# Kernel tuning notes

Hardware: AMD Instinct MI355X
Metric: run time of the kernel (lower is better)

The kernel has to match this reference:

```python
import jax, jax.numpy as jnp
import numpy as np

B, D, H, NL, DFF, N = 64, 768, 12, 12, 3072, 197
HD = D // H  # 64
SCALE = HD ** -0.5


def setup_inputs() -> dict:
    key = jax.random.key(0)
    ks = iter(jax.random.split(key, 64))
    def rn(shape, s=0.02):
        return jax.random.normal(next(ks), shape, jnp.float32) * s
    inp = {
        'x': jax.random.normal(next(ks), (B, 12, 1000), jnp.float32),
        # PatchEmbed convs (torch Conv1d weight layout OIH)
        'conv1_w': rn((256, 12, 5), 0.1), 'conv1_b': jnp.zeros((256,), jnp.float32),
        'bn1_g': jnp.ones((256,), jnp.float32), 'bn1_b': jnp.zeros((256,), jnp.float32),
        'bn1_m': jnp.zeros((256,), jnp.float32), 'bn1_v': jnp.ones((256,), jnp.float32),
        'conv2_w': rn((768, 256, 5), 0.05), 'conv2_b': jnp.zeros((768,), jnp.float32),
        'bn2_g': jnp.ones((768,), jnp.float32), 'bn2_b': jnp.zeros((768,), jnp.float32),
        'bn2_m': jnp.zeros((768,), jnp.float32), 'bn2_v': jnp.ones((768,), jnp.float32),
        'cls_token': rn((1, 1, D)), 'pos_embed': rn((1, N, D)),
        # 12 transformer blocks, stacked. Linear weights stored [in, out].
        'ln1_g': jnp.ones((NL, D), jnp.float32), 'ln1_b': jnp.zeros((NL, D), jnp.float32),
        'qkv_w': rn((NL, D, 3 * D)),            # qkv_bias=False
        'proj_w': rn((NL, D, D)), 'proj_b': jnp.zeros((NL, D), jnp.float32),
        'ln2_g': jnp.ones((NL, D), jnp.float32), 'ln2_b': jnp.zeros((NL, D), jnp.float32),
        'fc1_w': rn((NL, D, DFF)), 'fc1_b': jnp.zeros((NL, DFF), jnp.float32),
        'fc2_w': rn((NL, DFF, D)), 'fc2_b': jnp.zeros((NL, D), jnp.float32),
        'norm_g': jnp.ones((D,), jnp.float32), 'norm_b': jnp.zeros((D,), jnp.float32),
        # ProjectionHead (nonlinear): Linear(768->768,no bias)+BN, ReLU, Linear(768->512,no bias)+BN
        'p1_w': rn((D, D)),
        'p1bn_g': jnp.ones((D,), jnp.float32), 'p1bn_b': jnp.zeros((D,), jnp.float32),
        'p1bn_m': jnp.zeros((D,), jnp.float32), 'p1bn_v': jnp.ones((D,), jnp.float32),
        'p2_w': rn((D, 512)),
        'p2bn_g': jnp.ones((512,), jnp.float32), 'p2bn_b': jnp.zeros((512,), jnp.float32),
        'p2bn_m': jnp.zeros((512,), jnp.float32), 'p2bn_v': jnp.ones((512,), jnp.float32),
    }
    return inp


def _conv1d(x, w, b, stride):
    y = jax.lax.conv_general_dilated(x, w, (stride,), 'VALID',
                                     dimension_numbers=('NCH', 'OIH', 'NCH'))
    return y + b[None, :, None]


def _bn_c(x, g, b, m, v, eps=1e-5):  # BatchNorm1d eval, channel axis 1 of (B,C,L)
    return (x - m[None, :, None]) * (g[None, :, None] / jnp.sqrt(v[None, :, None] + eps)) + b[None, :, None]


def _bn_f(x, g, b, m, v, eps=1e-5):  # BatchNorm1d eval on (B,F)
    return (x - m) * (g / jnp.sqrt(v + eps)) + b


def _ln(x, g, b, eps=1e-6):
    mu = x.mean(-1, keepdims=True)
    var = jnp.var(x, axis=-1, keepdims=True)
    return (x - mu) * jax.lax.rsqrt(var + eps) * g + b


def reference(x, conv1_w, conv1_b, bn1_g, bn1_b, bn1_m, bn1_v,
              conv2_w, conv2_b, bn2_g, bn2_b, bn2_m, bn2_v,
              cls_token, pos_embed,
              ln1_g, ln1_b, qkv_w, proj_w, proj_b,
              ln2_g, ln2_b, fc1_w, fc1_b, fc2_w, fc2_b,
              norm_g, norm_b,
              p1_w, p1bn_g, p1bn_b, p1bn_m, p1bn_v,
              p2_w, p2bn_g, p2bn_b, p2bn_m, p2bn_v):
    # PatchEmbed: conv -> ReLU -> BN, twice; then (B, 196, 768)
    h = _bn_c(jax.nn.relu(_conv1d(x, conv1_w, conv1_b, 5)), bn1_g, bn1_b, bn1_m, bn1_v)
    h = _bn_c(jax.nn.relu(_conv1d(h, conv2_w, conv2_b, 1)), bn2_g, bn2_b, bn2_m, bn2_v)
    h = jnp.transpose(h, (0, 2, 1))  # [B, 196, D]
    b = h.shape[0]
    tok = jnp.concatenate([jnp.broadcast_to(cls_token, (b, 1, D)), h], axis=1) + pos_embed  # [B, 197, D]

    for i in range(NL):
        y = _ln(tok, ln1_g[i], ln1_b[i])
        qkv = jnp.einsum('bnd,de->bne', y, qkv_w[i]).reshape(b, N, 3, H, HD)
        q, k, v = jnp.moveaxis(qkv, 2, 0)  # each [B, N, H, HD]
        q = jnp.transpose(q, (0, 2, 1, 3)) * SCALE  # [B, H, N, HD]
        k = jnp.transpose(k, (0, 2, 1, 3))
        v = jnp.transpose(v, (0, 2, 1, 3))
        attn = jax.nn.softmax(jnp.einsum('bhnd,bhmd->bhnm', q, k), axis=-1)
        o = jnp.einsum('bhnm,bhmd->bhnd', attn, v)
        o = jnp.transpose(o, (0, 2, 1, 3)).reshape(b, N, D)
        tok = tok + jnp.einsum('bnd,de->bne', o, proj_w[i]) + proj_b[i]
        y = _ln(tok, ln2_g[i], ln2_b[i])
        y = jax.nn.gelu(jnp.einsum('bnd,df->bnf', y, fc1_w[i]) + fc1_b[i], approximate=False)
        tok = tok + jnp.einsum('bnf,fd->bnd', y, fc2_w[i]) + fc2_b[i]

    cls = _ln(tok, norm_g, norm_b)[:, 0]  # global_pool='token'
    z = _bn_f(cls @ p1_w, p1bn_g, p1bn_b, p1bn_m, p1bn_v)
    z = jax.nn.relu(z)
    z = _bn_f(z @ p2_w, p2bn_g, p2bn_b, p2bn_m, p2bn_v)
    return z
```

## Files before the change

### kernel.cpp

```cpp
#include <hip/hip_runtime.h>
#include <hip/hip_bf16.h>

typedef __hip_bfloat16 bf16;
typedef __attribute__((ext_vector_type(8))) short bf16x8;
typedef __attribute__((ext_vector_type(4))) float f32x4;

__device__ __forceinline__ float bf2f(bf16 v) { return __bfloat162float(v); }
__device__ __forceinline__ unsigned short f2bfu(float f) {
    bf16 h = __float2bfloat16(f);
    return __builtin_bit_cast(unsigned short, h);
}

__device__ __forceinline__ void gload16(const void* g, void* lds) {
    __builtin_amdgcn_global_load_lds(
        (const __attribute__((address_space(1))) unsigned int*)g,
        (__attribute__((address_space(3))) unsigned int*)lds, 16, 0, 0);
}

__device__ __forceinline__ float gelu_f(float x) {
    float u = 0.7978845608f * (x + 0.044715f * x * x * x);
    float e = __expf(-2.0f * fabsf(u));
    float th = (1.f - e) / (1.f + e);
    th = u < 0.f ? -th : th;
    return 0.5f * x * (1.f + th);
}

__global__ __launch_bounds__(256)
void conv1_kernel(const float* __restrict__ x, const float* __restrict__ w,
                  const float* __restrict__ bias,
                  const float* __restrict__ g, const float* __restrict__ b,
                  const float* __restrict__ m, const float* __restrict__ v,
                  bf16* __restrict__ h1) {
    int bo = blockIdx.x;
    int bb = bo >> 8, o = bo & 255;
    int l = threadIdx.x;
    if (l >= 200) return;
    const float* wo = w + o * 60;
    const float* xb = x + bb * 12000;
    float acc = bias[o];
#pragma unroll
    for (int i = 0; i < 12; i++)
#pragma unroll
        for (int t = 0; t < 5; t++)
            acc = fmaf(xb[i * 1000 + 5 * l + t], wo[i * 5 + t], acc);
    acc = fmaxf(acc, 0.f);
    float sc = g[o] * rsqrtf(v[o] + 1e-5f);
    acc = (acc - m[o]) * sc + b[o];
    h1[bo * 200 + l] = __float2bfloat16(acc);
}

__global__ __launch_bounds__(256)
void im2col_kernel(const bf16* __restrict__ h1, bf16* __restrict__ A2) {
    int idx = blockIdx.x * 256 + threadIdx.x;
    int row = idx / 1280, c = idx - row * 1280;
    int bb = row / 196, l = row - bb * 196;
    int i = c / 5, t = c - i * 5;
    A2[idx] = h1[(bb * 256 + i) * 200 + l + t];
}

__global__ __launch_bounds__(256)
void add_cls_pos(const float* __restrict__ cls, const float* __restrict__ pos,
                 float* __restrict__ tok) {
    int idx = blockIdx.x * 256 + threadIdx.x;
    int bb = idx / 768, d = idx - bb * 768;
    tok[(size_t)bb * 197 * 768 + d] = cls[d] + pos[d];
}

__global__ __launch_bounds__(256)
void cvt_kernel(const float* __restrict__ in, bf16* __restrict__ out, int n) {
    int idx = blockIdx.x * 256 + threadIdx.x;
    if (idx < n) out[idx] = __float2bfloat16(in[idx]);
}

__global__ __launch_bounds__(256)
void wtrans_layer(const float* __restrict__ qkvw, const float* __restrict__ projw,
                  const float* __restrict__ fc1w, const float* __restrict__ fc2w,
                  bf16* __restrict__ qkvT, bf16* __restrict__ projT,
                  bf16* __restrict__ fc1T, bf16* __restrict__ fc2T) {
    __shared__ float tile[32][33];
    int blk = blockIdx.x;
    const float* in; bf16* out; int Kd, Nd, t0;
    if (blk < 1728)      { in = qkvw; out = qkvT; Kd = 768;  Nd = 2304; t0 = blk; }
    else if (blk < 2304) { in = projw; out = projT; Kd = 768;  Nd = 768;  t0 = blk - 1728; }
    else if (blk < 4608) { in = fc1w; out = fc1T; Kd = 768;  Nd = 3072; t0 = blk - 2304; }
    else                 { in = fc2w; out = fc2T; Kd = 3072; Nd = 768;  t0 = blk - 4608; }
    int ntiles = Nd >> 5;
    int kt = t0 / ntiles, nt = t0 - kt * ntiles;
    int k0 = kt * 32, n0 = nt * 32;
    int tx = threadIdx.x & 31, ty = threadIdx.x >> 5;
#pragma unroll
    for (int j = 0; j < 4; j++)
        tile[ty + 8 * j][tx] = in[(size_t)(k0 + ty + 8 * j) * Nd + n0 + tx];
    __syncthreads();
#pragma unroll
    for (int j = 0; j < 4; j++)
        out[(size_t)(n0 + ty + 8 * j) * Kd + k0 + tx] = __float2bfloat16(tile[tx][ty + 8 * j]);
}

__global__ __launch_bounds__(256)
void wtrans2(const float* __restrict__ in, bf16* __restrict__ out, int Kd, int Nd) {
    __shared__ float tile[32][33];
    int ntiles = Nd >> 5;
    int kt = blockIdx.x / ntiles, nt = blockIdx.x - kt * ntiles;
    int k0 = kt * 32, n0 = nt * 32;
    int tx = threadIdx.x & 31, ty = threadIdx.x >> 5;
#pragma unroll
    for (int j = 0; j < 4; j++)
        tile[ty + 8 * j][tx] = in[(size_t)(k0 + ty + 8 * j) * Nd + n0 + tx];
    __syncthreads();
#pragma unroll
    for (int j = 0; j < 4; j++)
        out[(size_t)(n0 + ty + 8 * j) * Kd + k0 + tx] = __float2bfloat16(tile[tx][ty + 8 * j]);
}

__global__ __launch_bounds__(256)
void ln_kernel(const float* __restrict__ x, bf16* __restrict__ y,
               const float* __restrict__ g, const float* __restrict__ b,
               int nrows, int xstride) {
    int row = blockIdx.x * 4 + (threadIdx.x >> 6);
    if (row >= nrows) return;
    int l = threadIdx.x & 63;
    const float* xr = x + (size_t)row * xstride;
    float4 v0 = *(const float4*)(xr + l * 4);
    float4 v1 = *(const float4*)(xr + 256 + l * 4);
    float4 v2 = *(const float4*)(xr + 512 + l * 4);
    float s1 = 0.f, s2 = 0.f;
    {
        float e;
        e = v0.x; s1 += e; s2 += e * e;  e = v0.y; s1 += e; s2 += e * e;
        e = v0.z; s1 += e; s2 += e * e;  e = v0.w; s1 += e; s2 += e * e;
        e = v1.x; s1 += e; s2 += e * e;  e = v1.y; s1 += e; s2 += e * e;
        e = v1.z; s1 += e; s2 += e * e;  e = v1.w; s1 += e; s2 += e * e;
        e = v2.x; s1 += e; s2 += e * e;  e = v2.y; s1 += e; s2 += e * e;
        e = v2.z; s1 += e; s2 += e * e;  e = v2.w; s1 += e; s2 += e * e;
    }
#pragma unroll
    for (int off = 1; off < 64; off <<= 1) {
        s1 += __shfl_xor(s1, off);
        s2 += __shfl_xor(s2, off);
    }
    float mu = s1 * (1.f / 768.f);
    float rs = rsqrtf(s2 * (1.f / 768.f) - mu * mu + 1e-6f);
    bf16* yr = y + (size_t)row * 768;
#pragma unroll
    for (int sgi = 0; sgi < 3; sgi++) {
        float4 vv = sgi == 0 ? v0 : (sgi == 1 ? v1 : v2);
        float4 gg = *(const float4*)(g + sgi * 256 + l * 4);
        float4 bb = *(const float4*)(b + sgi * 256 + l * 4);
        ushort4 o;
        o.x = f2bfu((vv.x - mu) * rs * gg.x + bb.x);
        o.y = f2bfu((vv.y - mu) * rs * gg.y + bb.y);
        o.z = f2bfu((vv.z - mu) * rs * gg.z + bb.z);
        o.w = f2bfu((vv.w - mu) * rs * gg.w + bb.w);
        *(ushort4*)(yr + sgi * 256 + l * 4) = o;
    }
}

enum { E_BF16 = 0, E_RESID = 1, E_GELU = 2, E_CONV2 = 3, E_HEAD1 = 4, E_HEAD2 = 5 };

template<int EPI>
__global__ __launch_bounds__(256)
void gemm2(const bf16* __restrict__ A, const bf16* __restrict__ Bt,
           int M, int N, int K,
           const float* __restrict__ bias,
           bf16* __restrict__ Co, float* __restrict__ tok,
           const float* __restrict__ bng, const float* __restrict__ bnb,
           const float* __restrict__ bnm, const float* __restrict__ bnv,
           const float* __restrict__ pos) {
    __shared__ bf16 As[128 * 64];
    __shared__ bf16 Bs[128 * 64];
    const int t = threadIdx.x;
    const int l = t & 63, w = t >> 6;
    const int wm = (w >> 1) * 64, wn = (w & 1) * 64;

    const int gx = gridDim.x;
    const int nwg = gx * gridDim.y;
    const int d = blockIdx.y * gx + blockIdx.x;
    const int q = nwg >> 3, r = nwg & 7;
    const int xcd = d & 7, pos_ = d >> 3;
    const int lid = (xcd < r ? xcd * (q + 1) : r * (q + 1) + (xcd - r) * q) + pos_;
    const int row0 = (lid / gx) * 128, col0 = (lid % gx) * 128;

    const int lr = l & 15, kg = l >> 4;

    const int srow = w * 8 + (l >> 3);
    const int sc = ((l & 7) ^ (l >> 3)) * 8;
    const int dstoff = w * 1024 + l * 16;

    const f32x4 zero4 = {0.f, 0.f, 0.f, 0.f};
    f32x4 acc[4][4];
#pragma unroll
    for (int i = 0; i < 4; i++)
#pragma unroll
        for (int j = 0; j < 4; j++) acc[i][j] = zero4;

    for (int k0 = 0; k0 < K; k0 += 64) {
#pragma unroll
        for (int p = 0; p < 4; p++) {
            int rr = srow + p * 32;
            int gra = row0 + rr; if (gra >= M) gra = M - 1;
            gload16(A + (size_t)gra * K + k0 + sc, (char*)As + p * 4096 + dstoff);
            gload16(Bt + (size_t)(col0 + rr) * K + k0 + sc, (char*)Bs + p * 4096 + dstoff);
        }
        __syncthreads();
#pragma unroll
        for (int ks = 0; ks < 2; ks++) {
            bf16x8 af[4], bfv[4];
            const int cc = ((ks * 4 + kg) ^ (lr & 7)) * 16;
#pragma unroll
            for (int i = 0; i < 4; i++) {
                af[i]  = *(const bf16x8*)((const char*)As + (wm + i * 16 + lr) * 128 + cc);
                bfv[i] = *(const bf16x8*)((const char*)Bs + (wn + i * 16 + lr) * 128 + cc);
            }
#pragma unroll
            for (int i = 0; i < 4; i++)
#pragma unroll
                for (int j = 0; j < 4; j++)
                    acc[i][j] = __builtin_amdgcn_mfma_f32_16x16x32_bf16(af[i], bfv[j], acc[i][j], 0, 0, 0);
        }
        __syncthreads();
    }

    const int rbase = row0 + wm + (kg << 2);
#pragma unroll
    for (int i = 0; i < 4; i++) {
#pragma unroll
        for (int sr = 0; sr < 4; sr++) {
            int rr = rbase + i * 16 + sr;
            if (rr < M) {
#pragma unroll
                for (int j = 0; j < 4; j++) {
                    int c = col0 + wn + j * 16 + lr;
                    float vv = acc[i][j][sr];
                    if (EPI == E_BF16) {
                        Co[(size_t)rr * N + c] = __float2bfloat16(vv);
                    } else if (EPI == E_RESID) {
                        float* p = tok + (size_t)rr * N + c;
                        *p += vv + bias[c];
                    } else if (EPI == E_GELU) {
                        Co[(size_t)rr * N + c] = __float2bfloat16(gelu_f(vv + bias[c]));
                    } else if (EPI == E_CONV2) {
                        float xx = vv + bias[c];
                        xx = fmaxf(xx, 0.f);
                        float sc2 = bng[c] * rsqrtf(bnv[c] + 1e-5f);
                        xx = (xx - bnm[c]) * sc2 + bnb[c];
                        int bb = rr / 196, ll = rr - bb * 196;
                        xx += pos[(size_t)(1 + ll) * 768 + c];
                        tok[(size_t)(bb * 197 + 1 + ll) * 768 + c] = xx;
                    } else if (EPI == E_HEAD1) {
                        float sc2 = bng[c] * rsqrtf(bnv[c] + 1e-5f);
                        float xx = (vv - bnm[c]) * sc2 + bnb[c];
                        xx = fmaxf(xx, 0.f);
                        Co[(size_t)rr * N + c] = __float2bfloat16(xx);
                    } else {
                        float sc2 = bng[c] * rsqrtf(bnv[c] + 1e-5f);
                        tok[(size_t)rr * N + c] = (vv - bnm[c]) * sc2 + bnb[c];
                    }
                }
            }
        }
    }
}

#define ATTN_LDS (208 * 72 * 2 + 64 * 232 * 2 + 4 * 16 * 232 * 2)

__global__ __launch_bounds__(256)
void attn_kernel(const bf16* __restrict__ qkv, bf16* __restrict__ o) {
    extern __shared__ char smem[];
    bf16* Ks = (bf16*)smem;
    bf16* Vt = Ks + 208 * 72;
    bf16* Pl = Vt + 64 * 232;
    const int bh = blockIdx.x, bb = bh / 12, h = bh - bb * 12;
    const int t = threadIdx.x, w = t >> 6, l = t & 63;
    const int lr = l & 15, lk8 = (l >> 4) * 8;
    const size_t base = (size_t)bb * 197 * 2304 + (size_t)h * 64;

    for (int qi = t; qi < 197 * 16; qi += 256) {
        int n = qi >> 4, d4 = (qi & 15) << 2;
        ushort4 kv = *(const ushort4*)(qkv + base + (size_t)n * 2304 + 768 + d4);
        *(ushort4*)&Ks[n * 72 + d4] = kv;
    }
    for (int qi = t; qi < 11 * 72; qi += 256) ((unsigned short*)Ks)[197 * 72 + qi] = 0;
    for (int qi = t; qi < 197 * 16; qi += 256) {
        int n = qi >> 4, d4 = (qi & 15) << 2;
        ushort4 vv = *(const ushort4*)(qkv + base + (size_t)n * 2304 + 1536 + d4);
        ((unsigned short*)Vt)[(d4 + 0) * 232 + n] = vv.x;
        ((unsigned short*)Vt)[(d4 + 1) * 232 + n] = vv.y;
        ((unsigned short*)Vt)[(d4 + 2) * 232 + n] = vv.z;
        ((unsigned short*)Vt)[(d4 + 3) * 232 + n] = vv.w;
    }
    for (int qi = t; qi < 64 * 35; qi += 256) {
        int d = qi / 35, c = 197 + (qi - d * 35);
        ((unsigned short*)Vt)[d * 232 + c] = 0;
    }
    __syncthreads();

    bf16* Pw = Pl + w * (16 * 232);
    const f32x4 zero4 = {0.f, 0.f, 0.f, 0.f};
    for (int qt = w; qt < 13; qt += 4) {
        int m0 = qt * 16;
        int qrow = m0 + lr; if (qrow > 196) qrow = 196;
        const bf16* qp = qkv + (size_t)(bb * 197 + qrow) * 2304 + h * 64 + lk8;
        bf16x8 a0 = *(const bf16x8*)qp;
        bf16x8 a1 = *(const bf16x8*)(qp + 32);
        f32x4 s[13];
#pragma unroll
        for (int kt = 0; kt < 13; kt++) {
            const bf16* kp = &Ks[(kt * 16 + lr) * 72 + lk8];
            bf16x8 b0 = *(const bf16x8*)kp;
            bf16x8 b1 = *(const bf16x8*)(kp + 32);
            f32x4 z = zero4;
            z = __builtin_amdgcn_mfma_f32_16x16x32_bf16(a0, b0, z, 0, 0, 0);
            z = __builtin_amdgcn_mfma_f32_16x16x32_bf16(a1, b1, z, 0, 0, 0);
            s[kt] = z;
        }
        float mx[4] = {-1e30f, -1e30f, -1e30f, -1e30f};
#pragma unroll
        for (int kt = 0; kt < 13; kt++) {
            bool valid = (kt < 12) || (lr <= 4);
#pragma unroll
            for (int sr = 0; sr < 4; sr++) {
                float sv = s[kt][sr] * 0.125f;
                sv = valid ? sv : -1e30f;
                s[kt][sr] = sv;
                mx[sr] = fmaxf(mx[sr], sv);
            }
        }
#pragma unroll
        for (int off = 1; off < 16; off <<= 1)
#pragma unroll
            for (int sr = 0; sr < 4; sr++)
                mx[sr] = fmaxf(mx[sr], __shfl_xor(mx[sr], off));
        float sum[4] = {0.f, 0.f, 0.f, 0.f};
#pragma unroll
        for (int kt = 0; kt < 13; kt++)
#pragma unroll
            for (int sr = 0; sr < 4; sr++) {
                float p = __expf(s[kt][sr] - mx[sr]);
                s[kt][sr] = p;
                sum[sr] += p;
            }
#pragma unroll
        for (int off = 1; off < 16; off <<= 1)
#pragma unroll
            for (int sr = 0; sr < 4; sr++)
                sum[sr] += __shfl_xor(sum[sr], off);
        float inv[4];
#pragma unroll
        for (int sr = 0; sr < 4; sr++) inv[sr] = 1.f / sum[sr];
#pragma unroll
        for (int kt = 0; kt < 13; kt++)
#pragma unroll
            for (int sr = 0; sr < 4; sr++)
                ((unsigned short*)Pw)[((l >> 4) * 4 + sr) * 232 + kt * 16 + lr] =
                    f2bfu(s[kt][sr] * inv[sr]);
        for (int j = l; j < 256; j += 64) {
            int rr = j >> 4, cc = 208 + (j & 15);
            ((unsigned short*)Pw)[rr * 232 + cc] = 0;
        }
        asm volatile("s_waitcnt lgkmcnt(0)" ::: "memory");
        f32x4 oa[4];
#pragma unroll
        for (int nf = 0; nf < 4; nf++) oa[nf] = zero4;
#pragma unroll
        for (int ks = 0; ks < 7; ks++) {
            const bf16* pp = &Pw[lr * 232 + ks * 32 + lk8];
            bf16x8 ap = *(const bf16x8*)pp;
#pragma unroll
            for (int nf = 0; nf < 4; nf++) {
                bf16x8 bv = *(const bf16x8*)&Vt[(nf * 16 + lr) * 232 + ks * 32 + lk8];
                oa[nf] = __builtin_amdgcn_mfma_f32_16x16x32_bf16(ap, bv, oa[nf], 0, 0, 0);
            }
        }
#pragma unroll
        for (int nf = 0; nf < 4; nf++)
#pragma unroll
            for (int sr = 0; sr < 4; sr++) {
                int orow = m0 + (l >> 4) * 4 + sr;
                if (orow <= 196)
                    o[(size_t)(bb * 197 + orow) * 768 + h * 64 + nf * 16 + lr] =
                        __float2bfloat16(oa[nf][sr]);
            }
    }
}

extern "C" void kernel_launch(void* const* d_in, const int* in_sizes, int n_in,
                              void* d_out, int out_size, void* d_ws, size_t ws_size,
                              hipStream_t stream) {
    (void)in_sizes; (void)n_in; (void)out_size; (void)ws_size;
    const float* x        = (const float*)d_in[0];
    const float* conv1_w  = (const float*)d_in[1];
    const float* conv1_b  = (const float*)d_in[2];
    const float* bn1_g = (const float*)d_in[3],  *bn1_b = (const float*)d_in[4];
    const float* bn1_m = (const float*)d_in[5],  *bn1_v = (const float*)d_in[6];
    const float* conv2_w  = (const float*)d_in[7];
    const float* conv2_b  = (const float*)d_in[8];
    const float* bn2_g = (const float*)d_in[9],  *bn2_b = (const float*)d_in[10];
    const float* bn2_m = (const float*)d_in[11], *bn2_v = (const float*)d_in[12];
    const float* cls_tok  = (const float*)d_in[13];
    const float* pos      = (const float*)d_in[14];
    const float* ln1_g = (const float*)d_in[15], *ln1_b = (const float*)d_in[16];
    const float* qkv_w = (const float*)d_in[17];
    const float* proj_w = (const float*)d_in[18], *proj_b = (const float*)d_in[19];
    const float* ln2_g = (const float*)d_in[20], *ln2_b = (const float*)d_in[21];
    const float* fc1_w = (const float*)d_in[22], *fc1_b = (const float*)d_in[23];
    const float* fc2_w = (const float*)d_in[24], *fc2_b = (const float*)d_in[25];
    const float* norm_g = (const float*)d_in[26], *norm_b = (const float*)d_in[27];
    const float* p1_w = (const float*)d_in[28];
    const float* p1g = (const float*)d_in[29], *p1b = (const float*)d_in[30];
    const float* p1m = (const float*)d_in[31], *p1v = (const float*)d_in[32];
    const float* p2_w = (const float*)d_in[33];
    const float* p2g = (const float*)d_in[34], *p2b = (const float*)d_in[35];
    const float* p2m = (const float*)d_in[36], *p2v = (const float*)d_in[37];

    char* ws = (char*)d_ws;
    float* tok  = (float*)(ws + 0);
    bf16* ybf   = (bf16*)(ws + 38731776);
    bf16* qkvb  = (bf16*)(ws + 58097664);
    bf16* a1    = (bf16*)(ws + 116195328);
    bf16* h1    = (bf16*)(ws + 116195328);
    bf16* A2    = (bf16*)(ws + 116195328 + 8388608);
    bf16* clsb  = (bf16*)(ws + 193658880);
    bf16* z1    = (bf16*)(ws + 193757184);
    bf16* wtb   = (bf16*)(ws + 193953792);
    bf16* qkvT = wtb;
    bf16* projT = wtb + 1769472;
    bf16* fc1T = wtb + 2359296;
    bf16* fc2T = wtb + 4718592;
    bf16* conv2T = wtb;
    bf16* p1T = a1;
    bf16* p2T = a1 + 768 * 768;

    (void)hipFuncSetAttribute((const void*)attn_kernel,
                              hipFuncAttributeMaxDynamicSharedMemorySize, ATTN_LDS);

    conv1_kernel<<<64 * 256, 256, 0, stream>>>(x, conv1_w, conv1_b, bn1_g, bn1_b, bn1_m, bn1_v, h1);
    im2col_kernel<<<(12544 * 1280) / 256, 256, 0, stream>>>(h1, A2);
    cvt_kernel<<<(768 * 1280 + 255) / 256, 256, 0, stream>>>(conv2_w, conv2T, 768 * 1280);
    gemm2<E_CONV2><<<dim3(6, 98), 256, 0, stream>>>(
        A2, conv2T, 12544, 768, 1280, conv2_b, nullptr, tok, bn2_g, bn2_b, bn2_m, bn2_v, pos);
    add_cls_pos<<<(64 * 768) / 256, 256, 0, stream>>>(cls_tok, pos, tok);

    const int MT = (12608 + 127) / 128;
    for (int i = 0; i < 12; i++) {
        wtrans_layer<<<6912, 256, 0, stream>>>(
            qkv_w + (size_t)i * 768 * 2304, proj_w + (size_t)i * 768 * 768,
            fc1_w + (size_t)i * 768 * 3072, fc2_w + (size_t)i * 3072 * 768,
            qkvT, projT, fc1T, fc2T);
        ln_kernel<<<12608 / 4, 256, 0, stream>>>(tok, ybf, ln1_g + i * 768, ln1_b + i * 768, 12608, 768);
        gemm2<E_BF16><<<dim3(18, MT), 256, 0, stream>>>(
            ybf, qkvT, 12608, 2304, 768,
            nullptr, qkvb, nullptr, nullptr, nullptr, nullptr, nullptr, nullptr);
        attn_kernel<<<768, 256, ATTN_LDS, stream>>>(qkvb, ybf);
        gemm2<E_RESID><<<dim3(6, MT), 256, 0, stream>>>(
            ybf, projT, 12608, 768, 768,
            proj_b + i * 768, nullptr, tok, nullptr, nullptr, nullptr, nullptr, nullptr);
        ln_kernel<<<12608 / 4, 256, 0, stream>>>(tok, ybf, ln2_g + i * 768, ln2_b + i * 768, 12608, 768);
        gemm2<E_GELU><<<dim3(24, MT), 256, 0, stream>>>(
            ybf, fc1T, 12608, 3072, 768,
            fc1_b + i * 3072, a1, nullptr, nullptr, nullptr, nullptr, nullptr, nullptr);
        gemm2<E_RESID><<<dim3(6, MT), 256, 0, stream>>>(
            a1, fc2T, 12608, 768, 3072,
            fc2_b + i * 768, nullptr, tok, nullptr, nullptr, nullptr, nullptr, nullptr);
    }

    ln_kernel<<<16, 256, 0, stream>>>(tok, clsb, norm_g, norm_b, 64, 197 * 768);
    wtrans2<<<576, 256, 0, stream>>>(p1_w, p1T, 768, 768);
    wtrans2<<<384, 256, 0, stream>>>(p2_w, p2T, 768, 512);
    gemm2<E_HEAD1><<<dim3(6, 1), 256, 0, stream>>>(
        clsb, p1T, 64, 768, 768,
        nullptr, z1, nullptr, p1g, p1b, p1m, p1v, nullptr);
    gemm2<E_HEAD2><<<dim3(4, 1), 256, 0, stream>>>(
        z1, p2T, 64, 512, 768,
        nullptr, nullptr, (float*)d_out, p2g, p2b, p2m, p2v, nullptr);
}
```

Baseline: 4.883 ms.

## Add 256x256-tile 4-stage pipelined GEMM for QKV and FC1 projections

Introduces a new GEMM kernel with 256x256 output tiles, 512 threads, a 4-deep LDS ring buffer filled by direct global-to-LDS loads, XOR-swizzled LDS layout, and an XCD-aware block remapping. It replaces the previous 128-row GEMM for the QKV and FC1 (GELU) projections. The goal is more data reuse per tile, better overlap of loads with MFMA work, and better L2 locality per XCD. The cost is 128KB of LDS per block and high register pressure from 32 accumulator fragments per thread. A 256-row tile also wastes more padded rows at the M tail.

```diff
diff --git a/kernel.cpp b/kernel.cpp
--- a/kernel.cpp
+++ b/kernel.cpp
@@ -262,6 +262,129 @@
     }
 }
 
+#define G3_LDS 131072
+
+template<int EPI>
+__global__ __launch_bounds__(512, 2)
+void gemm3(const bf16* __restrict__ A, const bf16* __restrict__ Bt,
+           int M, int N, int K,
+           const float* __restrict__ bias, bf16* __restrict__ Co) {
+    extern __shared__ char smem[];
+    const int t = threadIdx.x;
+    const int l = t & 63, wid = t >> 6;
+    const int wr = wid >> 2, wc = wid & 3;
+    const int lr = l & 15, kg = l >> 4;
+
+    const int gx = gridDim.x;
+    const int nwg = gx * gridDim.y;
+    const int d = blockIdx.y * gx + blockIdx.x;
+    const int q = nwg >> 3, r = nwg & 7;
+    const int xcd = d & 7, pp = d >> 3;
+    const int lid = (xcd < r ? xcd * (q + 1) : r * (q + 1) + (xcd - r) * q) + pp;
+    const int row0 = (lid / gx) * 256, col0 = (lid % gx) * 256;
+
+    const int srow = t >> 2;
+    const int clog = ((t & 3) ^ (srow & 3)) * 8;
+    int ga0 = row0 + srow;        if (ga0 >= M) ga0 = M - 1;
+    int ga1 = row0 + 128 + srow;  if (ga1 >= M) ga1 = M - 1;
+    const bf16* Ap0 = A + (size_t)ga0 * K + clog;
+    const bf16* Ap1 = A + (size_t)ga1 * K + clog;
+    const bf16* Bp0 = Bt + (size_t)(col0 + srow) * K + clog;
+    const bf16* Bp1 = Bt + (size_t)(col0 + 128 + srow) * K + clog;
+    const int dst = t * 16;
+
+    const f32x4 zero4 = {0.f, 0.f, 0.f, 0.f};
+    f32x4 acc[8][4];
+#pragma unroll
+    for (int i = 0; i < 8; i++)
+#pragma unroll
+        for (int n = 0; n < 4; n++) acc[i][n] = zero4;
+
+    auto stage = [&](int j) {
+        char* base = smem + (j & 3) * 32768 + dst;
+        const int ke = j * 32;
+        gload16(Ap0 + ke, base);
+        gload16(Ap1 + ke, base + 8192);
+        gload16(Bp0 + ke, base + 16384);
+        gload16(Bp1 + ke, base + 16384 + 8192);
+    };
+
+    const int ccA = ((kg ^ (lr & 3)) * 16);
+    const int arow = (wr * 128 + lr) * 64 + ccA;
+    const int brow = (wc * 64 + lr) * 64 + ccA;
+
+    auto compute = [&](int j) {
+        const char* ab = smem + (j & 3) * 32768;
+        bf16x8 bfrag[4];
+#pragma unroll
+        for (int n = 0; n < 4; n++)
+            bfrag[n] = *(const bf16x8*)(ab + 16384 + brow + n * 1024);
+#pragma unroll
+        for (int mh = 0; mh < 2; mh++) {
+            bf16x8 af[4];
+#pragma unroll
+            for (int i2 = 0; i2 < 4; i2++)
+                af[i2] = *(const bf16x8*)(ab + arow + (mh * 4 + i2) * 1024);
+            __builtin_amdgcn_s_setprio(1);
+#pragma unroll
+            for (int i2 = 0; i2 < 4; i2++)
+#pragma unroll
+                for (int n = 0; n < 4; n++)
+                    acc[mh * 4 + i2][n] = __builtin_amdgcn_mfma_f32_16x16x32_bf16(
+                        af[i2], bfrag[n], acc[mh * 4 + i2][n], 0, 0, 0);
+            __builtin_amdgcn_s_setprio(0);
+        }
+    };
+
+    const int nt = K >> 5;
+    stage(0); stage(1); stage(2);
+
+    for (int j = 0; j < nt - 2; ++j) {
+        asm volatile("s_waitcnt vmcnt(8)\n\ts_waitcnt lgkmcnt(0)" ::: "memory");
+        __builtin_amdgcn_sched_barrier(0);
+        __builtin_amdgcn_s_barrier();
+        __builtin_amdgcn_sched_barrier(0);
+        if (j + 3 < nt) stage(j + 3);
+        compute(j);
+    }
+    {
+        asm volatile("s_waitcnt vmcnt(4)\n\ts_waitcnt lgkmcnt(0)" ::: "memory");
+        __builtin_amdgcn_sched_barrier(0);
+        __builtin_amdgcn_s_barrier();
+        __builtin_amdgcn_sched_barrier(0);
+        compute(nt - 2);
+    }
+    {
+        asm volatile("s_waitcnt vmcnt(0)\n\ts_waitcnt lgkmcnt(0)" ::: "memory");
+        __builtin_amdgcn_sched_barrier(0);
+        __builtin_amdgcn_s_barrier();
+        __builtin_amdgcn_sched_barrier(0);
+        compute(nt - 1);
+    }
+
+    float bs[4];
+#pragma unroll
+    for (int n = 0; n < 4; n++)
+        bs[n] = (EPI == E_GELU) ? bias[col0 + wc * 64 + n * 16 + lr] : 0.f;
+    const int rb = row0 + wr * 128 + kg * 4;
+    const int cb = col0 + wc * 64 + lr;
+#pragma unroll
+    for (int i = 0; i < 8; i++) {
+#pragma unroll
+        for (int sr = 0; sr < 4; sr++) {
+            int rr = rb + i * 16 + sr;
+            if (rr < M) {
+#pragma unroll
+                for (int n = 0; n < 4; n++) {
+                    float vv = acc[i][n][sr];
+                    if (EPI == E_GELU) vv = gelu_f(vv + bs[n]);
+                    Co[(size_t)rr * N + cb + n * 16] = __float2bfloat16(vv);
+                }
+            }
+        }
+    }
+}
+
 #define ATTN_LDS (208 * 72 * 2 + 64 * 232 * 2 + 4 * 16 * 232 * 2)
 
 __global__ __launch_bounds__(256)
@@ -433,6 +556,10 @@
 
     (void)hipFuncSetAttribute((const void*)attn_kernel,
                               hipFuncAttributeMaxDynamicSharedMemorySize, ATTN_LDS);
+    (void)hipFuncSetAttribute((const void*)gemm3<E_BF16>,
+                              hipFuncAttributeMaxDynamicSharedMemorySize, G3_LDS);
+    (void)hipFuncSetAttribute((const void*)gemm3<E_GELU>,
+                              hipFuncAttributeMaxDynamicSharedMemorySize, G3_LDS);
 
     conv1_kernel<<<64 * 256, 256, 0, stream>>>(x, conv1_w, conv1_b, bn1_g, bn1_b, bn1_m, bn1_v, h1);
     im2col_kernel<<<(12544 * 1280) / 256, 256, 0, stream>>>(h1, A2);
@@ -442,23 +569,22 @@
     add_cls_pos<<<(64 * 768) / 256, 256, 0, stream>>>(cls_tok, pos, tok);
 
     const int MT = (12608 + 127) / 128;
+    const int MT3 = (12608 + 255) / 256;
     for (int i = 0; i < 12; i++) {
         wtrans_layer<<<6912, 256, 0, stream>>>(
             qkv_w + (size_t)i * 768 * 2304, proj_w + (size_t)i * 768 * 768,
             fc1_w + (size_t)i * 768 * 3072, fc2_w + (size_t)i * 3072 * 768,
             qkvT, projT, fc1T, fc2T);
         ln_kernel<<<12608 / 4, 256, 0, stream>>>(tok, ybf, ln1_g + i * 768, ln1_b + i * 768, 12608, 768);
-        gemm2<E_BF16><<<dim3(18, MT), 256, 0, stream>>>(
-            ybf, qkvT, 12608, 2304, 768,
-            nullptr, qkvb, nullptr, nullptr, nullptr, nullptr, nullptr, nullptr);
+        gemm3<E_BF16><<<dim3(9, MT3), 512, G3_LDS, stream>>>(
+            ybf, qkvT, 12608, 2304, 768, nullptr, qkvb);
         attn_kernel<<<768, 256, ATTN_LDS, stream>>>(qkvb, ybf);
         gemm2<E_RESID><<<dim3(6, MT), 256, 0, stream>>>(
             ybf, projT, 12608, 768, 768,
             proj_b + i * 768, nullptr, tok, nullptr, nullptr, nullptr, nullptr, nullptr);
         ln_kernel<<<12608 / 4, 256, 0, stream>>>(tok, ybf, ln2_g + i * 768, ln2_b + i * 768, 12608, 768);
-        gemm2<E_GELU><<<dim3(24, MT), 256, 0, stream>>>(
-            ybf, fc1T, 12608, 3072, 768,
-            fc1_b + i * 3072, a1, nullptr, nullptr, nullptr, nullptr, nullptr, nullptr);
+        gemm3<E_GELU><<<dim3(12, MT3), 512, G3_LDS, stream>>>(
+            ybf, fc1T, 12608, 3072, 768, fc1_b + i * 3072, a1);
         gemm2<E_RESID><<<dim3(6, MT), 256, 0, stream>>>(
             a1, fc2T, 12608, 768, 3072,
             fc2_b + i * 768, nullptr, tok, nullptr, nullptr, nullptr, nullptr, nullptr);
```

Measured after the change: 4.738 ms. 3.0% less time.
